# Optimization experiments

Hardware: AMD Instinct MI355X
Metric: run time of the kernel (lower is better)

Reference implementation:

```python
import jax, jax.numpy as jnp
import numpy as np

B, N, D = 16, 1024, 16  # graphs, nodes, embedding_dim


def setup_inputs() -> dict:
    key = jax.random.key(0)
    ks = jax.random.split(key, 13)
    s = 0.05  # small weight scale to keep exp(alpha) well-behaved
    return {
        "X": jax.random.normal(ks[0], (B, N, D), dtype=jnp.float32),
        "init_param": jax.random.normal(ks[1], (2,), dtype=jnp.float32) * s,
        "Wq": jax.random.normal(ks[2], (D - 1, D, D), dtype=jnp.float32) * s,
        "bq": jax.random.normal(ks[3], (D - 1, D), dtype=jnp.float32) * s,
        "Wk": jax.random.normal(ks[4], (D - 1, D, D), dtype=jnp.float32) * s,
        "bk": jax.random.normal(ks[5], (D - 1, D), dtype=jnp.float32) * s,
        "Wv": jax.random.normal(ks[6], (D - 1, D, D), dtype=jnp.float32) * s,
        "bv": jax.random.normal(ks[7], (D - 1, D), dtype=jnp.float32) * s,
        "Wo": jax.random.normal(ks[8], (D - 1, D, D), dtype=jnp.float32) * s,
        "bo": jax.random.normal(ks[9], (D - 1, D), dtype=jnp.float32) * s,
        "Wf": jax.random.normal(ks[10], (D - 1, 2, D), dtype=jnp.float32) * s,
        "bf": jax.random.normal(ks[11], (D - 1, 2), dtype=jnp.float32) * s,
    }


def reference(X, init_param, Wq, bq, Wk, bk, Wv, bv, Wo, bo, Wf, bf):
    b, n, d = X.shape
    dt = X.dtype
    Zs = []
    logdet = jnp.zeros((b, n), dt)
    for i in range(d):
        if i == 0:
            mu, alpha = init_param[0], init_param[1]
        else:
            l = i - 1
            Xi = X[:, :, :i]  # [B,N,i] growing ragged slice
            Q = Xi @ Wq[l, :i, :i].T + bq[l, :i]
            K = Xi @ Wk[l, :i, :i].T + bk[l, :i]
            V = Xi @ Wv[l, :i, :i].T + bv[l, :i]
            # SAB/MAB: softmax(QK^T / sqrt(dim_V=i)); num_heads=1
            A = jax.nn.softmax(
                jnp.einsum("bnd,bmd->bnm", Q, K) / jnp.sqrt(jnp.asarray(i, dt)),
                axis=-1,
            )  # [B,N,N]
            O = Q + jnp.einsum("bnm,bmd->bnd", A, V)
            O = O + jax.nn.relu(O @ Wo[l, :i, :i].T + bo[l, :i])
            out = O @ Wf[l, :, :i].T + bf[l]  # [B,N,2]
            mu, alpha = out[..., 0], out[..., 1]
        Zs.append((X[:, :, i] - mu) / jnp.exp(alpha))
        logdet = logdet - alpha
    Z = jnp.stack(Zs, axis=-1)
    return Z, logdet
```

## Files before the change

### kernel.cpp

```cpp
#include <hip/hip_runtime.h>
#include <math.h>

#define Bb 16
#define Nn 1024
#define Dd 16
#define NL 15

typedef __attribute__((ext_vector_type(8))) short short8;
typedef __attribute__((ext_vector_type(16))) float f32x16;
typedef __attribute__((ext_vector_type(4))) unsigned uint4v;

#if __has_builtin(__builtin_amdgcn_exp2f)
#define EXP2(x) __builtin_amdgcn_exp2f(x)
#else
#define EXP2(x) exp2f(x)
#endif

#define PROJ_SZ ((size_t)NL * Bb * 1024 * 16)
#define WS_NEED (3 * PROJ_SZ * 2 + 1088 * 2)

#define VSTR 1040
#define V_OFF 32768
#define ONES_OFF 66048
#define RS_OFF 69632
#define LDS_TOTAL 73728

__device__ __forceinline__ unsigned pack2bf(float a, float b) {
    unsigned ua = __float_as_uint(a) + 0x8000u;
    unsigned ub = __float_as_uint(b) + 0x8000u;
    return (ua >> 16) | (ub & 0xffff0000u);
}
__device__ __forceinline__ unsigned short bf1(float a) {
    return (unsigned short)((__float_as_uint(a) + 0x8000u) >> 16);
}

__device__ __forceinline__ unsigned expperm(float x, float y) {
    unsigned ex = __float_as_uint(EXP2(x));
    unsigned ey = __float_as_uint(EXP2(y));
#if __has_builtin(__builtin_amdgcn_perm)
    return __builtin_amdgcn_perm(ey, ex, 0x07060302);
#else
    return (ex >> 16) | (ey & 0xffff0000u);
#endif
}

__device__ __forceinline__ int vperm(int m) {
    return (m & 3) + ((m & 8) >> 1) + ((m & 4) << 1);
}

__device__ __forceinline__ void project(const float* __restrict__ xrow,
                                        const float* __restrict__ W,
                                        const float* __restrict__ bias,
                                        int i, float* __restrict__ q) {
#pragma unroll
    for (int r = 0; r < 16; r++) q[r] = 0.f;
    for (int c = 0; c < i; c++) {
        float xc = xrow[c];
#pragma unroll
        for (int r = 0; r < 16; r++) q[r] = fmaf(xc, W[r * 16 + c], q[r]);
    }
#pragma unroll
    for (int r = 0; r < 16; r++) q[r] = (r < i) ? (q[r] + bias[r]) : 0.f;
}

__device__ __forceinline__ void load_row16(const float* __restrict__ p, float* __restrict__ x) {
    const float4* xp = (const float4*)p;
    float4 a = xp[0], b = xp[1], c = xp[2], d = xp[3];
    x[0]=a.x; x[1]=a.y; x[2]=a.z; x[3]=a.w;
    x[4]=b.x; x[5]=b.y; x[6]=b.z; x[7]=b.w;
    x[8]=c.x; x[9]=c.y; x[10]=c.z; x[11]=c.w;
    x[12]=d.x; x[13]=d.y; x[14]=d.z; x[15]=d.w;
}

__global__ void gf_init(const float* __restrict__ X, const float* __restrict__ ip,
                        float* __restrict__ out, unsigned short* __restrict__ onesb) {
    int idx = blockIdx.x * blockDim.x + threadIdx.x;
    if (idx >= Bb * Nn) return;
    if (onesb && idx < 1088) onesb[idx] = 0x3F80;
    float mu = ip[0], alpha = ip[1];
    float x0 = X[(size_t)idx * Dd];
    out[(size_t)idx * Dd] = (x0 - mu) * __expf(-alpha);
    out[(size_t)Bb * Nn * Dd + idx] = -alpha;
}

__global__ void gf_proj(const float* __restrict__ X,
                        const float* __restrict__ Wq, const float* __restrict__ bq,
                        const float* __restrict__ Wk, const float* __restrict__ bk,
                        const float* __restrict__ Wv, const float* __restrict__ bv,
                        unsigned short* __restrict__ Kg,
                        unsigned short* __restrict__ Vg,
                        unsigned short* __restrict__ Qg) {
    __shared__ unsigned short Vt[16 * 1040];
    const int l = blockIdx.x, b = blockIdx.y, i = l + 1;
    const int t = threadIdx.x;
    const size_t lb = (size_t)(l * Bb + b);
    const float qscale = 1.4426950408889634f * rsqrtf((float)i);

    const float* Xb  = X  + (size_t)b * Nn * Dd;
    const float* wq  = Wq + l * 256;  const float* bql = bq + l * 16;
    const float* wk  = Wk + l * 256;  const float* bkl = bk + l * 16;
    const float* wvp = Wv + l * 256;  const float* bvl = bv + l * 16;

    float xr[16]; load_row16(Xb + (size_t)t * Dd, xr);
    float tmp[16];

    project(xr, wk, bkl, i, tmp);
    {
        unsigned u[8];
#pragma unroll
        for (int r = 0; r < 8; r++) u[r] = pack2bf(tmp[2*r], tmp[2*r+1]);
        uint4* kd = (uint4*)(Kg + (lb * 1024 + t) * 16);
        kd[0] = make_uint4(u[0], u[1], u[2], u[3]);
        kd[1] = make_uint4(u[4], u[5], u[6], u[7]);
    }

    project(xr, wvp, bvl, i, tmp);
    {
        const int col = (t & ~15) + vperm(t & 15);
#pragma unroll
        for (int d = 0; d < 16; d++) Vt[d * 1040 + col] = bf1(tmp[d]);
    }

    project(xr, wq, bql, i, tmp);
    {
        unsigned u[8];
#pragma unroll
        for (int r = 0; r < 8; r++) u[r] = pack2bf(tmp[2*r] * qscale, tmp[2*r+1] * qscale);
        uint4* qd = (uint4*)(Qg + (lb * 1024 + t) * 16);
        qd[0] = make_uint4(u[0], u[1], u[2], u[3]);
        qd[1] = make_uint4(u[4], u[5], u[6], u[7]);
    }

    __syncthreads();
    {
        const int d = t >> 6, seg = t & 63;
        const uint4* src = (const uint4*)(Vt + d * 1040 + seg * 16);
        uint4* dst = (uint4*)(Vg + lb * (16 * 1024) + d * 1024 + seg * 16);
        dst[0] = src[0];
        dst[1] = src[1];
    }
}

__launch_bounds__(256, 4)
__global__ void gf_attn(const float* __restrict__ X,
                        const unsigned short* __restrict__ Kg,
                        const unsigned short* __restrict__ Vg,
                        const unsigned short* __restrict__ Qg,
                        const unsigned short* __restrict__ onesb,
                        const float* __restrict__ Wo, const float* __restrict__ bo,
                        const float* __restrict__ Wf, const float* __restrict__ bf,
                        float* __restrict__ out) {
    __shared__ float Osh[4 * 32 * 17];
    __shared__ float Rsh[4 * 32];

    const int bx = blockIdx.x;
    const int c = bx & 7, k = bx >> 3;
    const int G = c * 30 + (k >> 3);
    const int z = k & 7;
    const int l = G % NL, b = G / NL, i = l + 1;

    const int t = threadIdx.x;
    const int wid = t >> 6, lane = t & 63;
    const int q31 = lane & 31, h = lane >> 5;
    const size_t lb = (size_t)(l * Bb + b);
    const int qbase = z * 128 + wid * 32;

    short8 qf = *(const short8*)(Qg + (lb * 1024 + qbase + q31) * 16 + 8 * h);

    const unsigned short* Kp = Kg + (lb * 1024 + q31) * 16 + 8 * h;
    const unsigned short* Vp = ((q31 < 16) ? (Vg + (lb * 16 + q31) * 1024)
                                           : onesb) + 8 * h;

    const f32x16 zf16 = {};
    f32x16 D = {};

    short8 kf_in, vc0, vc1, vn0, vn1;
    f32x16 s_cur;
    {
        short8 k0 = *(const short8*)Kp;
        vc0 = *(const short8*)(Vp);
        vc1 = *(const short8*)(Vp + 16);
        s_cur = __builtin_amdgcn_mfma_f32_32x32x16_bf16(k0, qf, zf16, 0, 0, 0);
        kf_in = *(const short8*)(Kp + 32 * 16);
        vn0 = *(const short8*)(Vp + 32);
        vn1 = *(const short8*)(Vp + 48);
    }

    for (int lk = 0; lk < Nn; lk += 32) {
        const int kn = (lk + 64) & (Nn - 1);
        short8 kf2 = *(const short8*)(Kp + (size_t)kn * 16);
        short8 w0  = *(const short8*)(Vp + kn);
        short8 w1  = *(const short8*)(Vp + kn + 16);

        f32x16 s_nxt = __builtin_amdgcn_mfma_f32_32x32x16_bf16(kf_in, qf, zf16, 0, 0, 0);

        {
            uint4v a0 = {expperm(s_cur[0], s_cur[1]), expperm(s_cur[2], s_cur[3]),
                         expperm(s_cur[4], s_cur[5]), expperm(s_cur[6], s_cur[7])};
            D = __builtin_amdgcn_mfma_f32_32x32x16_bf16(
                    __builtin_bit_cast(short8, a0), vc0, D, 0, 0, 0);
        }
        {
            uint4v a1 = {expperm(s_cur[8], s_cur[9]),  expperm(s_cur[10], s_cur[11]),
                         expperm(s_cur[12], s_cur[13]), expperm(s_cur[14], s_cur[15])};
            D = __builtin_amdgcn_mfma_f32_32x32x16_bf16(
                    __builtin_bit_cast(short8, a1), vc1, D, 0, 0, 0);
        }

        s_cur = s_nxt;
        kf_in = kf2;
        vc0 = vn0; vc1 = vn1;
        vn0 = w0;  vn1 = w1;
    }

    float* Ow = Osh + wid * (32 * 17);
    if (q31 < 16) {
#pragma unroll
        for (int r = 0; r < 16; r++) {
            int m = (r & 3) + 8 * (r >> 2) + 4 * h;
            Ow[m * 17 + q31] = D[r];
        }
    }
    if (q31 == 16) {
        float* Rw = Rsh + wid * 32;
#pragma unroll
        for (int r = 0; r < 16; r++) {
            int m = (r & 3) + 8 * (r >> 2) + 4 * h;
            Rw[m] = D[r];
        }
    }
    __syncthreads();

    if (t < 128) {
        const int qn = z * 128 + t;
        const float invq = 0.6931471805599453f * sqrtf((float)i);

        float a[16];
        {
            const uint4* qp = (const uint4*)(Qg + (lb * 1024 + qn) * 16);
            uint4 u0 = qp[0], u1 = qp[1];
            unsigned uw[8] = {u0.x, u0.y, u0.z, u0.w, u1.x, u1.y, u1.z, u1.w};
#pragma unroll
            for (int r = 0; r < 8; r++) {
                a[2*r]     = __uint_as_float(uw[r] << 16) * invq;
                a[2*r + 1] = __uint_as_float(uw[r] & 0xffff0000u) * invq;
            }
        }

        const float* orow = Osh + (t >> 5) * (32 * 17) + (t & 31) * 17;
        const float  inv  = 1.f / Rsh[(t >> 5) * 32 + (t & 31)];
#pragma unroll
        for (int cc = 0; cc < 16; cc++) a[cc] += orow[cc] * inv;

        const float* wo  = Wo + l * 256;  const float* bol = bo + l * 16;
        const float* wf  = Wf + l * 32;   const float* bfl = bf + l * 2;

        float tt[16];
#pragma unroll
        for (int r = 0; r < 16; r++) {
            float acc = bol[r];
#pragma unroll
            for (int cc = 0; cc < 16; cc++) acc = fmaf(a[cc], wo[r * 16 + cc], acc);
            tt[r] = fmaxf(acc, 0.f);
        }
#pragma unroll
        for (int r = 0; r < 16; r++) a[r] += (r < i) ? tt[r] : 0.f;

        float mu = bfl[0], al = bfl[1];
#pragma unroll
        for (int cc = 0; cc < 16; cc++) {
            mu = fmaf(a[cc], wf[cc], mu);
            al = fmaf(a[cc], wf[16 + cc], al);
        }
        const float xi = X[((size_t)b * Nn + qn) * Dd + i];
        out[((size_t)(b * Nn + qn)) * Dd + i] = (xi - mu) * __expf(-al);
        atomicAdd(out + (size_t)Bb * Nn * Dd + b * Nn + qn, -al);
    }
}

__launch_bounds__(1024, 4)
__global__ void gf_fused(const float* __restrict__ X,
                         const float* __restrict__ Wq, const float* __restrict__ bq,
                         const float* __restrict__ Wk, const float* __restrict__ bk,
                         const float* __restrict__ Wv, const float* __restrict__ bv,
                         const float* __restrict__ Wo, const float* __restrict__ bo,
                         const float* __restrict__ Wf, const float* __restrict__ bf,
                         float* __restrict__ out) {
    extern __shared__ char smem[];
    const int l = blockIdx.x, b = blockIdx.y, i = l + 1;
    const int t = threadIdx.x;
    const int wid = t >> 6, lane = t & 63;
    const int q31 = lane & 31, h = lane >> 5;
    const float qscale = 1.4426950408889634f * rsqrtf((float)i);

    unsigned short* Ksh  = (unsigned short*)smem;
    unsigned short* Vsh  = (unsigned short*)(smem + V_OFF);
    unsigned short* Ones = (unsigned short*)(smem + ONES_OFF);

    const float* Xb  = X  + (size_t)b * Nn * Dd;
    const float* wq  = Wq + l * 256;  const float* bql = bq + l * 16;
    const float* wk  = Wk + l * 256;  const float* bkl = bk + l * 16;
    const float* wvp = Wv + l * 256;  const float* bvl = bv + l * 16;
    const float* wo  = Wo + l * 256;  const float* bol = bo + l * 16;
    const float* wf  = Wf + l * 32;   const float* bfl = bf + l * 2;

    unsigned qu[8];
    {
        float xr[16]; load_row16(Xb + (size_t)t * Dd, xr);
        float tmp[16];

        project(xr, wk, bkl, i, tmp);
        {
            unsigned u[8];
#pragma unroll
            for (int r = 0; r < 8; r++) u[r] = pack2bf(tmp[2*r], tmp[2*r+1]);
            uint4* kd = (uint4*)(Ksh + t * 16);
            kd[0] = make_uint4(u[0], u[1], u[2], u[3]);
            kd[1] = make_uint4(u[4], u[5], u[6], u[7]);
        }

        project(xr, wvp, bvl, i, tmp);
        {
            unsigned short* vcol = Vsh + (t & ~15) + vperm(t & 15);
#pragma unroll
            for (int d = 0; d < 16; d++) vcol[d * VSTR] = bf1(tmp[d]);
        }

        Ones[t] = 0x3F80;

        project(xr, wq, bql, i, tmp);
#pragma unroll
        for (int r = 0; r < 8; r++) qu[r] = pack2bf(tmp[2*r] * qscale, tmp[2*r+1] * qscale);
    }
    __syncthreads();

    short8 qf0, qf1;
    {
        unsigned d0[4], d1[4];
#pragma unroll
        for (int j = 0; j < 4; j++) {
            unsigned lo = __shfl(qu[j], q31);
            unsigned hi = __shfl(qu[4 + j], q31);
            d0[j] = h ? hi : lo;
            lo = __shfl(qu[j], 32 + q31);
            hi = __shfl(qu[4 + j], 32 + q31);
            d1[j] = h ? hi : lo;
        }
        uint4v v0 = {d0[0], d0[1], d0[2], d0[3]};
        uint4v v1 = {d1[0], d1[1], d1[2], d1[3]};
        qf0 = __builtin_bit_cast(short8, v0);
        qf1 = __builtin_bit_cast(short8, v1);
    }

    f32x16 zf16 = {};
    f32x16 D0 = {}, D1 = {};

    const unsigned short* Kp = Ksh + (size_t)q31 * 16 + h * 8;
    const unsigned short* Vp = ((q31 < 16) ? (Vsh + (size_t)q31 * VSTR) : Ones) + 8 * h;

    short8 kf  = *(const short8*)Kp;
    short8 vc0 = *(const short8*)(Vp);
    short8 vc1 = *(const short8*)(Vp + 16);

    for (int kb = 0; kb < Nn; kb += 32) {
        const int kn = (kb + 32) & (Nn - 1);
        short8 kfn = *(const short8*)(Kp + (size_t)kn * 16);
        short8 vn0 = *(const short8*)(Vp + kn);
        short8 vn1 = *(const short8*)(Vp + kn + 16);

        f32x16 s0 = __builtin_amdgcn_mfma_f32_32x32x16_bf16(kf, qf0, zf16, 0, 0, 0);
        f32x16 s1 = __builtin_amdgcn_mfma_f32_32x32x16_bf16(kf, qf1, zf16, 0, 0, 0);
        kf = kfn;

        {
            uint4v a0 = {expperm(s0[0], s0[1]), expperm(s0[2], s0[3]),
                         expperm(s0[4], s0[5]), expperm(s0[6], s0[7])};
            D0 = __builtin_amdgcn_mfma_f32_32x32x16_bf16(
                     __builtin_bit_cast(short8, a0), vc0, D0, 0, 0, 0);
            uint4v a1 = {expperm(s1[0], s1[1]), expperm(s1[2], s1[3]),
                         expperm(s1[4], s1[5]), expperm(s1[6], s1[7])};
            D1 = __builtin_amdgcn_mfma_f32_32x32x16_bf16(
                     __builtin_bit_cast(short8, a1), vc0, D1, 0, 0, 0);
        }
        {
            uint4v a0 = {expperm(s0[8], s0[9]),  expperm(s0[10], s0[11]),
                         expperm(s0[12], s0[13]), expperm(s0[14], s0[15])};
            D0 = __builtin_amdgcn_mfma_f32_32x32x16_bf16(
                     __builtin_bit_cast(short8, a0), vc1, D0, 0, 0, 0);
            uint4v a1 = {expperm(s1[8], s1[9]),  expperm(s1[10], s1[11]),
                         expperm(s1[12], s1[13]), expperm(s1[14], s1[15])};
            D1 = __builtin_amdgcn_mfma_f32_32x32x16_bf16(
                     __builtin_bit_cast(short8, a1), vc1, D1, 0, 0, 0);
        }
        vc0 = vn0; vc1 = vn1;
    }

    __syncthreads();

    float* Ow = (float*)smem + wid * (64 * 17);
    if (q31 < 16) {
#pragma unroll
        for (int r = 0; r < 16; r++) {
            int m = (r & 3) + 8 * (r >> 2) + 4 * h;
            Ow[m * 17 + q31]        = D0[r];
            Ow[(m + 32) * 17 + q31] = D1[r];
        }
    }
    float* Rw = (float*)(smem + RS_OFF) + wid * 64;
    if (q31 == 16) {
#pragma unroll
        for (int r = 0; r < 16; r++) {
            int m = (r & 3) + 8 * (r >> 2) + 4 * h;
            Rw[m]      = D0[r];
            Rw[32 + m] = D1[r];
        }
    }

    {
        const float invq = 0.6931471805599453f * sqrtf((float)i);

        float a[16];
#pragma unroll
        for (int r = 0; r < 8; r++) {
            a[2*r]     = __uint_as_float(qu[r] << 16) * invq;
            a[2*r + 1] = __uint_as_float(qu[r] & 0xffff0000u) * invq;
        }

        const float* orow = (const float*)smem + wid * (64 * 17) + lane * 17;
        const float  inv  = 1.f / Rw[lane];
#pragma unroll
        for (int c = 0; c < 16; c++) a[c] += orow[c] * inv;

        float tt[16];
#pragma unroll
        for (int r = 0; r < 16; r++) {
            float acc = bol[r];
#pragma unroll
            for (int c = 0; c < 16; c++) acc = fmaf(a[c], wo[r * 16 + c], acc);
            tt[r] = fmaxf(acc, 0.f);
        }
#pragma unroll
        for (int r = 0; r < 16; r++) a[r] += (r < i) ? tt[r] : 0.f;

        float mu = bfl[0], al = bfl[1];
#pragma unroll
        for (int c = 0; c < 16; c++) {
            mu = fmaf(a[c], wf[c], mu);
            al = fmaf(a[c], wf[16 + c], al);
        }
        const float xi = Xb[(size_t)t * Dd + i];
        out[((size_t)(b * Nn + t)) * Dd + i] = (xi - mu) * __expf(-al);
        atomicAdd(out + (size_t)Bb * Nn * Dd + b * Nn + t, -al);
    }
}

__launch_bounds__(512, 2)
__global__ void gf_layer_fb(const float* __restrict__ X,
                            const float* __restrict__ Wq, const float* __restrict__ bq,
                            const float* __restrict__ Wk, const float* __restrict__ bk,
                            const float* __restrict__ Wv, const float* __restrict__ bv,
                            const float* __restrict__ Wo, const float* __restrict__ bo,
                            const float* __restrict__ Wf, const float* __restrict__ bf,
                            float* __restrict__ out) {
    const int l = blockIdx.x, b = blockIdx.y, i = l + 1, t = threadIdx.x;
    const float rscale = rsqrtf((float)i);
    __shared__ float Ksh[512 * 16];
    __shared__ float Vsh[512 * 16];
    const float* Xb = X + (size_t)b * Nn * Dd;
    const float* wq = Wq + l * 256; const float* wk = Wk + l * 256;
    const float* wv = Wv + l * 256; const float* wo = Wo + l * 256;
    const float* wf = Wf + l * 32;
    const float* bql = bq + l * 16; const float* bkl = bk + l * 16;
    const float* bvl = bv + l * 16; const float* bol = bo + l * 16;
    const float* bfl = bf + l * 2;
    const int n0 = t, n1 = t + 512;
    float q0[16], q1[16], xi0, xi1;
    {
        float xr[16];
        load_row16(Xb + (size_t)n0 * Dd, xr); xi0 = xr[i]; project(xr, wq, bql, i, q0);
        load_row16(Xb + (size_t)n1 * Dd, xr); xi1 = xr[i]; project(xr, wq, bql, i, q1);
    }
    float o0[16], o1[16];
#pragma unroll
    for (int c = 0; c < 16; c++) { o0[c] = 0.f; o1[c] = 0.f; }
    float ls0 = 0.f, ls1 = 0.f;
    for (int ch = 0; ch < 2; ch++) {
        float kr[16], vr[16];
        {
            float kx[16];
            load_row16(Xb + (size_t)(ch * 512 + t) * Dd, kx);
            project(kx, wk, bkl, i, kr);
            project(kx, wv, bvl, i, vr);
        }
        __syncthreads();
#pragma unroll
        for (int j = 0; j < 4; j++) {
            ((float4*)&Ksh[t * 16])[j] = ((float4*)kr)[j];
            ((float4*)&Vsh[t * 16])[j] = ((float4*)vr)[j];
        }
        __syncthreads();
        for (int k = 0; k < 512; k++) {
            float kk[16], vv[16];
#pragma unroll
            for (int j = 0; j < 4; j++) ((float4*)kk)[j] = ((const float4*)&Ksh[k * 16])[j];
            float s0 = 0.f, s1 = 0.f;
#pragma unroll
            for (int c = 0; c < 16; c++) { s0 = fmaf(q0[c], kk[c], s0); s1 = fmaf(q1[c], kk[c], s1); }
            float p0 = __expf(s0 * rscale), p1 = __expf(s1 * rscale);
            ls0 += p0; ls1 += p1;
#pragma unroll
            for (int j = 0; j < 4; j++) ((float4*)vv)[j] = ((const float4*)&Vsh[k * 16])[j];
#pragma unroll
            for (int c = 0; c < 16; c++) { o0[c] = fmaf(p0, vv[c], o0[c]); o1[c] = fmaf(p1, vv[c], o1[c]); }
        }
        __syncthreads();
    }
    float* logdet = out + (size_t)Bb * Nn * Dd;
#pragma unroll
    for (int rowsel = 0; rowsel < 2; rowsel++) {
        const float* qr = rowsel ? q1 : q0; const float* orr = rowsel ? o1 : o0;
        float lsum = rowsel ? ls1 : ls0; float xin = rowsel ? xi1 : xi0;
        int n = rowsel ? n1 : n0;
        float a[16]; float inv = 1.f / lsum;
#pragma unroll
        for (int c = 0; c < 16; c++) a[c] = qr[c] + orr[c] * inv;
        float tt[16];
#pragma unroll
        for (int r = 0; r < 16; r++) {
            float acc = bol[r];
#pragma unroll
            for (int c = 0; c < 16; c++) acc = fmaf(a[c], wo[r * 16 + c], acc);
            tt[r] = fmaxf(acc, 0.f);
        }
#pragma unroll
        for (int r = 0; r < 16; r++) a[r] += (r < i) ? tt[r] : 0.f;
        float mu = bfl[0], al = bfl[1];
#pragma unroll
        for (int c = 0; c < 16; c++) { mu = fmaf(a[c], wf[c], mu); al = fmaf(a[c], wf[16 + c], al); }
        out[((size_t)(b * Nn + n)) * Dd + i] = (xin - mu) * __expf(-al);
        atomicAdd(logdet + b * Nn + n, -al);
    }
}

extern "C" void kernel_launch(void* const* d_in, const int* in_sizes, int n_in,
                              void* d_out, int out_size, void* d_ws, size_t ws_size,
                              hipStream_t stream) {
    const float* X  = (const float*)d_in[0];
    const float* ip = (const float*)d_in[1];
    const float* Wq = (const float*)d_in[2];
    const float* bq = (const float*)d_in[3];
    const float* Wk = (const float*)d_in[4];
    const float* bk = (const float*)d_in[5];
    const float* Wv = (const float*)d_in[6];
    const float* bv = (const float*)d_in[7];
    const float* Wo = (const float*)d_in[8];
    const float* bo = (const float*)d_in[9];
    const float* Wf = (const float*)d_in[10];
    const float* bf = (const float*)d_in[11];
    float* out = (float*)d_out;

    if (ws_size >= WS_NEED && d_ws != nullptr) {
        unsigned short* Kg    = (unsigned short*)d_ws;
        unsigned short* Vg    = Kg + PROJ_SZ;
        unsigned short* Qg    = Vg + PROJ_SZ;
        unsigned short* onesb = Qg + PROJ_SZ;

        gf_init<<<(Bb * Nn + 255) / 256, 256, 0, stream>>>(X, ip, out, onesb);
        gf_proj<<<dim3(NL, Bb), 1024, 0, stream>>>(X, Wq, bq, Wk, bk, Wv, bv,
                                                   Kg, Vg, Qg);
        gf_attn<<<NL * Bb * 8, 256, 0, stream>>>(X, Kg, Vg, Qg, onesb,
                                                 Wo, bo, Wf, bf, out);
        return;
    }

    gf_init<<<(Bb * Nn + 255) / 256, 256, 0, stream>>>(X, ip, out, nullptr);

    hipError_t e = hipFuncSetAttribute((const void*)gf_fused,
                                       hipFuncAttributeMaxDynamicSharedMemorySize,
                                       LDS_TOTAL);
    if (e == hipSuccess) {
        gf_fused<<<dim3(NL, Bb), 1024, LDS_TOTAL, stream>>>(
            X, Wq, bq, Wk, bk, Wv, bv, Wo, bo, Wf, bf, out);
    } else {
        gf_layer_fb<<<dim3(NL, Bb), 512, 0, stream>>>(
            X, Wq, bq, Wk, bk, Wv, bv, Wo, bo, Wf, bf, out);
    }
}
```

Before: 164.2 us.

## Fuse init into projection, split proj blocks, hand-pipeline attention loads

Folds the gf_init work (first output column, logdet init, ones buffer) into gf_proj, removing one kernel launch. It also splits gf_proj into two 512-thread halves per (layer, batch) to get more blocks. The attention loop now issues raw global_load_dwordx4 with explicit vmcnt waits and is unrolled by two. It uses two independent accumulators to break the MFMA dependency chain. The hand-written waits and inline asm risk stalls or ordering mistakes if the counts do not match what the compiler emits.

```diff
diff --git a/kernel.cpp b/kernel.cpp
--- a/kernel.cpp
+++ b/kernel.cpp
@@ -48,6 +48,14 @@
     return (m & 3) + ((m & 8) >> 1) + ((m & 4) << 1);
 }
 
+__device__ __forceinline__ uint4v gld16(const void* p) {
+    uint4v r;
+    asm volatile("global_load_dwordx4 %0, %1, off" : "=v"(r) : "v"(p));
+    return r;
+}
+#define WAITV3() do { asm volatile("s_waitcnt vmcnt(3)" ::: "memory"); \
+                      __builtin_amdgcn_sched_barrier(0); } while (0)
+
 __device__ __forceinline__ void project(const float* __restrict__ xrow,
                                         const float* __restrict__ W,
                                         const float* __restrict__ bias,
@@ -73,26 +81,28 @@
 }
 
 __global__ void gf_init(const float* __restrict__ X, const float* __restrict__ ip,
-                        float* __restrict__ out, unsigned short* __restrict__ onesb) {
+                        float* __restrict__ out) {
     int idx = blockIdx.x * blockDim.x + threadIdx.x;
     if (idx >= Bb * Nn) return;
-    if (onesb && idx < 1088) onesb[idx] = 0x3F80;
     float mu = ip[0], alpha = ip[1];
     float x0 = X[(size_t)idx * Dd];
     out[(size_t)idx * Dd] = (x0 - mu) * __expf(-alpha);
     out[(size_t)Bb * Nn * Dd + idx] = -alpha;
 }
 
-__global__ void gf_proj(const float* __restrict__ X,
+__global__ void gf_proj(const float* __restrict__ X, const float* __restrict__ ip,
                         const float* __restrict__ Wq, const float* __restrict__ bq,
                         const float* __restrict__ Wk, const float* __restrict__ bk,
                         const float* __restrict__ Wv, const float* __restrict__ bv,
                         unsigned short* __restrict__ Kg,
                         unsigned short* __restrict__ Vg,
-                        unsigned short* __restrict__ Qg) {
-    __shared__ unsigned short Vt[16 * 1040];
-    const int l = blockIdx.x, b = blockIdx.y, i = l + 1;
+                        unsigned short* __restrict__ Qg,
+                        unsigned short* __restrict__ onesb,
+                        float* __restrict__ out) {
+    __shared__ unsigned short Vt[16 * 520];
+    const int l = blockIdx.x, b = blockIdx.y, z = blockIdx.z, i = l + 1;
     const int t = threadIdx.x;
+    const int n = z * 512 + t;
     const size_t lb = (size_t)(l * Bb + b);
     const float qscale = 1.4426950408889634f * rsqrtf((float)i);
 
@@ -101,7 +111,7 @@
     const float* wk  = Wk + l * 256;  const float* bkl = bk + l * 16;
     const float* wvp = Wv + l * 256;  const float* bvl = bv + l * 16;
 
-    float xr[16]; load_row16(Xb + (size_t)t * Dd, xr);
+    float xr[16]; load_row16(Xb + (size_t)n * Dd, xr);
     float tmp[16];
 
     project(xr, wk, bkl, i, tmp);
@@ -109,7 +119,7 @@
         unsigned u[8];
 #pragma unroll
         for (int r = 0; r < 8; r++) u[r] = pack2bf(tmp[2*r], tmp[2*r+1]);
-        uint4* kd = (uint4*)(Kg + (lb * 1024 + t) * 16);
+        uint4* kd = (uint4*)(Kg + (lb * 1024 + n) * 16);
         kd[0] = make_uint4(u[0], u[1], u[2], u[3]);
         kd[1] = make_uint4(u[4], u[5], u[6], u[7]);
     }
@@ -118,7 +128,7 @@
     {
         const int col = (t & ~15) + vperm(t & 15);
 #pragma unroll
-        for (int d = 0; d < 16; d++) Vt[d * 1040 + col] = bf1(tmp[d]);
+        for (int d = 0; d < 16; d++) Vt[d * 520 + col] = bf1(tmp[d]);
     }
 
     project(xr, wq, bql, i, tmp);
@@ -126,16 +136,26 @@
         unsigned u[8];
 #pragma unroll
         for (int r = 0; r < 8; r++) u[r] = pack2bf(tmp[2*r] * qscale, tmp[2*r+1] * qscale);
-        uint4* qd = (uint4*)(Qg + (lb * 1024 + t) * 16);
+        uint4* qd = (uint4*)(Qg + (lb * 1024 + n) * 16);
         qd[0] = make_uint4(u[0], u[1], u[2], u[3]);
         qd[1] = make_uint4(u[4], u[5], u[6], u[7]);
     }
 
+    if (l == 0) {
+        const float mu = ip[0], al = ip[1];
+        out[((size_t)(b * Nn + n)) * Dd] = (xr[0] - mu) * __expf(-al);
+        out[(size_t)Bb * Nn * Dd + b * Nn + n] = -al;
+        if (b == 0 && z == 0) {
+            onesb[t] = 0x3F80; onesb[512 + t] = 0x3F80;
+            if (t < 64) onesb[1024 + t] = 0x3F80;
+        }
+    }
+
     __syncthreads();
     {
-        const int d = t >> 6, seg = t & 63;
-        const uint4* src = (const uint4*)(Vt + d * 1040 + seg * 16);
-        uint4* dst = (uint4*)(Vg + lb * (16 * 1024) + d * 1024 + seg * 16);
+        const int d = t >> 5, seg = t & 31;
+        const uint4* src = (const uint4*)(Vt + d * 520 + seg * 16);
+        uint4* dst = (uint4*)(Vg + lb * (16 * 1024) + d * 1024 + z * 512 + seg * 16);
         dst[0] = src[0];
         dst[1] = src[1];
     }
@@ -154,9 +174,9 @@
     __shared__ float Rsh[4 * 32];
 
     const int bx = blockIdx.x;
-    const int c = bx & 7, k = bx >> 3;
-    const int G = c * 30 + (k >> 3);
-    const int z = k & 7;
+    const int c8 = bx & 7, kk = bx >> 3;
+    const int G = c8 * 30 + (kk >> 3);
+    const int z = kk & 7;
     const int l = G % NL, b = G / NL, i = l + 1;
 
     const int t = threadIdx.x;
@@ -172,45 +192,73 @@
                                            : onesb) + 8 * h;
 
     const f32x16 zf16 = {};
-    f32x16 D = {};
-
-    short8 kf_in, vc0, vc1, vn0, vn1;
-    f32x16 s_cur;
-    {
-        short8 k0 = *(const short8*)Kp;
-        vc0 = *(const short8*)(Vp);
-        vc1 = *(const short8*)(Vp + 16);
-        s_cur = __builtin_amdgcn_mfma_f32_32x32x16_bf16(k0, qf, zf16, 0, 0, 0);
-        kf_in = *(const short8*)(Kp + 32 * 16);
-        vn0 = *(const short8*)(Vp + 32);
-        vn1 = *(const short8*)(Vp + 48);
-    }
-
-    for (int lk = 0; lk < Nn; lk += 32) {
-        const int kn = (lk + 64) & (Nn - 1);
-        short8 kf2 = *(const short8*)(Kp + (size_t)kn * 16);
-        short8 w0  = *(const short8*)(Vp + kn);
-        short8 w1  = *(const short8*)(Vp + kn + 16);
-
-        f32x16 s_nxt = __builtin_amdgcn_mfma_f32_32x32x16_bf16(kf_in, qf, zf16, 0, 0, 0);
-
-        {
-            uint4v a0 = {expperm(s_cur[0], s_cur[1]), expperm(s_cur[2], s_cur[3]),
-                         expperm(s_cur[4], s_cur[5]), expperm(s_cur[6], s_cur[7])};
-            D = __builtin_amdgcn_mfma_f32_32x32x16_bf16(
-                    __builtin_bit_cast(short8, a0), vc0, D, 0, 0, 0);
-        }
-        {
-            uint4v a1 = {expperm(s_cur[8], s_cur[9]),  expperm(s_cur[10], s_cur[11]),
-                         expperm(s_cur[12], s_cur[13]), expperm(s_cur[14], s_cur[15])};
-            D = __builtin_amdgcn_mfma_f32_32x32x16_bf16(
-                    __builtin_bit_cast(short8, a1), vc1, D, 0, 0, 0);
-        }
-
-        s_cur = s_nxt;
-        kf_in = kf2;
-        vc0 = vn0; vc1 = vn1;
-        vn0 = w0;  vn1 = w1;
+    f32x16 D0 = {}, D1 = {};
+    f32x16 s_cur, s_nxt;
+
+    uint4v k0u, k1u, v00u, v01u, v10u, v11u;
+
+    k0u  = gld16(Kp);
+    v00u = gld16(Vp);
+    v01u = gld16(Vp + 16);
+    k1u  = gld16(Kp + 32 * 16);
+    v10u = gld16(Vp + 32);
+    v11u = gld16(Vp + 48);
+    WAITV3();
+    s_cur = __builtin_amdgcn_mfma_f32_32x32x16_bf16(
+                __builtin_bit_cast(short8, k0u), qf, zf16, 0, 0, 0);
+
+#pragma unroll 1
+    for (int c = 0; c < 32; c += 2) {
+        {
+            const int kn2 = ((c + 2) << 5) & (Nn - 1);
+            k0u = gld16(Kp + (size_t)kn2 * 16);
+            WAITV3();
+            s_nxt = __builtin_amdgcn_mfma_f32_32x32x16_bf16(
+                        __builtin_bit_cast(short8, k1u), qf, zf16, 0, 0, 0);
+            {
+                uint4v a0 = {expperm(s_cur[0], s_cur[1]), expperm(s_cur[2], s_cur[3]),
+                             expperm(s_cur[4], s_cur[5]), expperm(s_cur[6], s_cur[7])};
+                D0 = __builtin_amdgcn_mfma_f32_32x32x16_bf16(
+                         __builtin_bit_cast(short8, a0),
+                         __builtin_bit_cast(short8, v00u), D0, 0, 0, 0);
+            }
+            {
+                uint4v a1 = {expperm(s_cur[8], s_cur[9]),  expperm(s_cur[10], s_cur[11]),
+                             expperm(s_cur[12], s_cur[13]), expperm(s_cur[14], s_cur[15])};
+                D1 = __builtin_amdgcn_mfma_f32_32x32x16_bf16(
+                         __builtin_bit_cast(short8, a1),
+                         __builtin_bit_cast(short8, v01u), D1, 0, 0, 0);
+            }
+            v00u = gld16(Vp + kn2);
+            v01u = gld16(Vp + kn2 + 16);
+            WAITV3();
+            s_cur = s_nxt;
+        }
+        {
+            const int kn2 = ((c + 3) << 5) & (Nn - 1);
+            k1u = gld16(Kp + (size_t)kn2 * 16);
+            WAITV3();
+            s_nxt = __builtin_amdgcn_mfma_f32_32x32x16_bf16(
+                        __builtin_bit_cast(short8, k0u), qf, zf16, 0, 0, 0);
+            {
+                uint4v a0 = {expperm(s_cur[0], s_cur[1]), expperm(s_cur[2], s_cur[3]),
+                             expperm(s_cur[4], s_cur[5]), expperm(s_cur[6], s_cur[7])};
+                D0 = __builtin_amdgcn_mfma_f32_32x32x16_bf16(
+                         __builtin_bit_cast(short8, a0),
+                         __builtin_bit_cast(short8, v10u), D0, 0, 0, 0);
+            }
+            {
+                uint4v a1 = {expperm(s_cur[8], s_cur[9]),  expperm(s_cur[10], s_cur[11]),
+                             expperm(s_cur[12], s_cur[13]), expperm(s_cur[14], s_cur[15])};
+                D1 = __builtin_amdgcn_mfma_f32_32x32x16_bf16(
+                         __builtin_bit_cast(short8, a1),
+                         __builtin_bit_cast(short8, v11u), D1, 0, 0, 0);
+            }
+            v10u = gld16(Vp + kn2);
+            v11u = gld16(Vp + kn2 + 16);
+            WAITV3();
+            s_cur = s_nxt;
+        }
     }
 
     float* Ow = Osh + wid * (32 * 17);
@@ -218,7 +266,7 @@
 #pragma unroll
         for (int r = 0; r < 16; r++) {
             int m = (r & 3) + 8 * (r >> 2) + 4 * h;
-            Ow[m * 17 + q31] = D[r];
+            Ow[m * 17 + q31] = D0[r] + D1[r];
         }
     }
     if (q31 == 16) {
@@ -226,7 +274,7 @@
 #pragma unroll
         for (int r = 0; r < 16; r++) {
             int m = (r & 3) + 8 * (r >> 2) + 4 * h;
-            Rw[m] = D[r];
+            Rw[m] = D0[r] + D1[r];
         }
     }
     __syncthreads();
@@ -565,15 +613,14 @@
         unsigned short* Qg    = Vg + PROJ_SZ;
         unsigned short* onesb = Qg + PROJ_SZ;
 
-        gf_init<<<(Bb * Nn + 255) / 256, 256, 0, stream>>>(X, ip, out, onesb);
-        gf_proj<<<dim3(NL, Bb), 1024, 0, stream>>>(X, Wq, bq, Wk, bk, Wv, bv,
-                                                   Kg, Vg, Qg);
+        gf_proj<<<dim3(NL, Bb, 2), 512, 0, stream>>>(X, ip, Wq, bq, Wk, bk, Wv, bv,
+                                                     Kg, Vg, Qg, onesb, out);
         gf_attn<<<NL * Bb * 8, 256, 0, stream>>>(X, Kg, Vg, Qg, onesb,
                                                  Wo, bo, Wf, bf, out);
         return;
     }
 
-    gf_init<<<(Bb * Nn + 255) / 256, 256, 0, stream>>>(X, ip, out, nullptr);
+    gf_init<<<(Bb * Nn + 255) / 256, 256, 0, stream>>>(X, ip, out);
 
     hipError_t e = hipFuncSetAttribute((const void*)gf_fused,
                                        hipFuncAttributeMaxDynamicSharedMemorySize,
```

Measured after the change: 160.4 us. 1.02x faster.
